# Kernel optimization log

Measured on AMD Instinct MI355X. Metric: run time of the kernel, lower is better.

## Reference

```python
import jax, jax.numpy as jnp
import numpy as np

WH, WW = 8, 8
N_TOK = WH * WW
NUM_HEADS = 4
DIM = 128
B_WIN = 4096  # num_windows * B
NW = 64       # windows per image (for mask)


def _make_rel_tables():
    # relative coords table (1, 2*Wh-1, 2*Ww-1, 2), log-spaced as in SwinV2
    ch = np.arange(-(WH - 1), WH, dtype=np.float32)
    cw = np.arange(-(WW - 1), WW, dtype=np.float32)
    t = np.stack(np.meshgrid(ch, cw, indexing='ij'), axis=-1)[None]  # (1,15,15,2)
    t[..., 0] /= (WH - 1)
    t[..., 1] /= (WW - 1)
    t *= 8
    t = np.sign(t) * np.log2(np.abs(t) + 1.0) / np.log2(8)
    # relative position index (N, N)
    coords = np.stack(np.meshgrid(np.arange(WH), np.arange(WW), indexing='ij'))
    cf = coords.reshape(2, -1)
    rel = cf[:, :, None] - cf[:, None, :]
    rel = rel.transpose(1, 2, 0).copy()
    rel[:, :, 0] += WH - 1
    rel[:, :, 1] += WW - 1
    rel[:, :, 0] *= 2 * WW - 1
    idx = rel.sum(-1).astype(np.int32)
    return jnp.asarray(t), jnp.asarray(idx)


def setup_inputs() -> dict:
    key = jax.random.key(0)
    ks = jax.random.split(key, 8)
    table, idx = _make_rel_tables()
    return {
        'x': jax.random.normal(ks[0], (B_WIN, N_TOK, DIM), jnp.float32),
        'context': jax.random.normal(ks[1], (B_WIN, N_TOK, DIM), jnp.float32),
        'mask': jnp.zeros((NW, N_TOK, N_TOK), jnp.float32),
        'q_w': jax.random.normal(ks[2], (DIM, DIM), jnp.float32) * 0.02,
        'q_b': jnp.zeros((DIM,), jnp.float32),
        'kv_w': jax.random.normal(ks[3], (2 * DIM, DIM), jnp.float32) * 0.02,
        'v_b': jnp.zeros((DIM,), jnp.float32),
        'logit_scale': jnp.full((NUM_HEADS, 1, 1), np.log(10.0), jnp.float32),
        'cpb_w1': jax.random.normal(ks[4], (512, 2), jnp.float32) * 0.02,
        'cpb_b1': jnp.zeros((512,), jnp.float32),
        'cpb_w2': jax.random.normal(ks[5], (NUM_HEADS, 512), jnp.float32) * 0.02,
        'proj_w': jax.random.normal(ks[6], (DIM, DIM), jnp.float32) * 0.02,
        'proj_b': jnp.zeros((DIM,), jnp.float32),
        'rel_coords_table': table,
        'rel_pos_index': idx,
    }


def _l2norm(t, eps=1e-12):
    return t / jnp.maximum(jnp.linalg.norm(t, axis=-1, keepdims=True), eps)


def reference(x, context, mask, q_w, q_b, kv_w, v_b, logit_scale,
              cpb_w1, cpb_b1, cpb_w2, proj_w, proj_b,
              rel_coords_table, rel_pos_index):
    B_, N, C = x.shape
    H = NUM_HEADS
    hd = C // H
    # projections (kv bias = [zeros_like(v_b); v_b])
    q = x @ q_w.T + q_b
    kv_bias = jnp.concatenate([jnp.zeros_like(v_b), v_b])
    kv = context @ kv_w.T + kv_bias
    q = q.reshape(B_, N, H, hd).transpose(0, 2, 1, 3)          # (B_,H,N,hd)
    kv = kv.reshape(B_, N, 2, H, hd).transpose(2, 0, 3, 1, 4)  # (2,B_,H,N,hd)
    k, v = kv[0], kv[1]
    # cosine attention with clamped learned scale
    attn = jnp.einsum('bhnd,bhmd->bhnm', _l2norm(q), _l2norm(k))
    scale = jnp.exp(jnp.minimum(logit_scale, np.log(1.0 / 0.01)))  # (H,1,1)
    attn = attn * scale[None]
    # CPB-MLP relative position bias
    hidd = jax.nn.relu(rel_coords_table @ cpb_w1.T + cpb_b1)   # (1,15,15,512)
    table = (hidd @ cpb_w2.T).reshape(-1, H)                   # ((2Wh-1)(2Ww-1), H)
    bias = table[rel_pos_index.reshape(-1)].reshape(N, N, H)
    bias = 16.0 * jax.nn.sigmoid(bias.transpose(2, 0, 1))      # (H,N,N)
    attn = attn + bias[None]
    # shift mask
    nW = mask.shape[0]
    attn = attn.reshape(B_ // nW, nW, H, N, N) + mask[None, :, None]
    attn = attn.reshape(B_, H, N, N)
    attn = jax.nn.softmax(attn, axis=-1)
    out = jnp.einsum('bhnm,bhmd->bhnd', attn, v)
    out = out.transpose(0, 2, 1, 3).reshape(B_, N, C)
    return out @ proj_w.T + proj_b
```

## Files before the change

kernel.cpp:

```cpp
#include <hip/hip_runtime.h>
#include <hip/hip_bf16.h>

#define NT 64
#define DIM 128
#define NH 4
#define HD 32

typedef __attribute__((ext_vector_type(8))) short short8;
typedef __attribute__((ext_vector_type(4))) short short4v;
typedef __attribute__((ext_vector_type(8))) __bf16 bf16x8;
typedef __attribute__((ext_vector_type(4))) float floatx4;

__device__ __forceinline__ short f2bf(float f) {
  unsigned u = __builtin_bit_cast(unsigned, f);
  u += 0x7FFFu + ((u >> 16) & 1u);
  return (short)(u >> 16);
}

__device__ __forceinline__ bf16x8 ldsfrag(const short* p) {
  return __builtin_bit_cast(bf16x8, *(const short8*)p);
}

#define MFMA(a,b,c) __builtin_amdgcn_mfma_f32_16x16x32_bf16(a,b,c,0,0,0)

__global__ void prep_kernel(const float* __restrict__ table,
                            const float* __restrict__ w1,
                            const float* __restrict__ b1,
                            const float* __restrict__ w2,
                            const int*   __restrict__ idx,
                            const float* __restrict__ q_w,
                            const float* __restrict__ kv_w,
                            const float* __restrict__ proj_w,
                            float* __restrict__ bias_packed,
                            short* __restrict__ wbf) {
  int t = threadIdx.x;
  if (blockIdx.x == 0) {
    __shared__ float logits[225][4];
    if (t < 225) {
      float t0 = table[2*t], t1 = table[2*t+1];
      float a0=0.f, a1=0.f, a2=0.f, a3=0.f;
      for (int j = 0; j < 512; ++j) {
        float h = fmaxf(0.f, t0 * w1[2*j] + t1 * w1[2*j+1] + b1[j]);
        a0 += h * w2[j];
        a1 += h * w2[512 + j];
        a2 += h * w2[1024 + j];
        a3 += h * w2[1536 + j];
      }
      logits[t][0]=a0; logits[t][1]=a1; logits[t][2]=a2; logits[t][3]=a3;
    }
    __syncthreads();
    for (int f = t; f < 16384; f += 256) {
      int i    = f & 3;
      int lane = (f >> 2) & 63;
      int nt   = (f >> 8) & 3;
      int mt   = (f >> 10) & 3;
      int h    = (f >> 12) & 3;
      int r = mt*16 + (lane >> 4)*4 + i;
      int c = nt*16 + (lane & 15);
      int p = idx[r*64 + c];
      float v = logits[p][h];
      bias_packed[f] = 16.f / (1.f + __expf(-v));
    }
  } else {
    int gidx = (blockIdx.x - 1) * 4096 + t * 16;
    const float* src; int off;
    if (gidx < 16384)      { src = q_w;    off = gidx; }
    else if (gidx < 49152) { src = kv_w;   off = gidx - 16384; }
    else                   { src = proj_w; off = gidx - 49152; }
    const float4* s = (const float4*)(src + off);
    short* dst = wbf + gidx;
#pragma unroll
    for (int i = 0; i < 2; ++i) {
      float4 a = s[2*i], b = s[2*i+1];
      short8 v;
      v[0]=f2bf(a.x); v[1]=f2bf(a.y); v[2]=f2bf(a.z); v[3]=f2bf(a.w);
      v[4]=f2bf(b.x); v[5]=f2bf(b.y); v[6]=f2bf(b.z); v[7]=f2bf(b.w);
      *(short8*)(dst + i*8) = v;
    }
  }
}

__global__ __launch_bounds__(512, 4)
void swin_ctx_attn_kernel(const float* __restrict__ x, const float* __restrict__ ctx,
                          const float* __restrict__ mask,
                          const short* __restrict__ wq, const float* __restrict__ q_b,
                          const short* __restrict__ wkv, const float* __restrict__ v_b,
                          const float* __restrict__ logit_scale,
                          const short* __restrict__ wproj, const float* __restrict__ proj_b,
                          const float* __restrict__ bias_p,
                          float* __restrict__ out) {
  __shared__ short lds[38400] __attribute__((aligned(16)));
  const int tid  = threadIdx.x;
  const int lane = tid & 63;
  const int wv   = tid >> 6;
  const int h    = wv >> 1;
  const int s    = wv & 1;
  const int b    = blockIdx.x;
  const int lr   = lane & 15;
  const int lg   = lane >> 4;

  short* stage = lds;
  short* hb    = lds + 8704 + h * 7424;
  short* qn    = hb;
  short* kn    = hb + 2560;
  short* attnb = hb;
  short* vT    = hb + 5120;

  const int sr = tid >> 3, sc = (tid & 7) * 16;
  {
    const float4* sx = (const float4*)(x + (size_t)b * (NT*DIM) + sr*DIM + sc);
    short* d = stage + sr*136 + sc;
#pragma unroll
    for (int i = 0; i < 2; ++i) {
      float4 a = sx[2*i], bb = sx[2*i+1];
      short8 v;
      v[0]=f2bf(a.x); v[1]=f2bf(a.y); v[2]=f2bf(a.z); v[3]=f2bf(a.w);
      v[4]=f2bf(bb.x); v[5]=f2bf(bb.y); v[6]=f2bf(bb.z); v[7]=f2bf(bb.w);
      *(short8*)(d + i*8) = v;
    }
  }
  float4 cr[4];
  {
    const float4* cs = (const float4*)(ctx + (size_t)b * (NT*DIM) + sr*DIM + sc);
#pragma unroll
    for (int i = 0; i < 4; ++i) cr[i] = cs[i];
  }
  __syncthreads();

  {
    floatx4 acc[2][2] = {};
    for (int ks = 0; ks < 4; ++ks) {
      bf16x8 A[2];
#pragma unroll
      for (int m = 0; m < 2; ++m)
        A[m] = ldsfrag(stage + (s*32 + m*16 + lr)*136 + ks*32 + lg*8);
#pragma unroll
      for (int nt = 0; nt < 2; ++nt) {
        bf16x8 B = ldsfrag(wq + (h*32 + nt*16 + lr)*DIM + ks*32 + lg*8);
#pragma unroll
        for (int m = 0; m < 2; ++m)
          acc[m][nt] = MFMA(A[m], B, acc[m][nt]);
      }
    }
    float qb0 = q_b[h*32 + lr], qb1 = q_b[h*32 + 16 + lr];
#pragma unroll
    for (int m = 0; m < 2; ++m) {
      floatx4 ss;
#pragma unroll
      for (int i = 0; i < 4; ++i) {
        acc[m][0][i] += qb0; acc[m][1][i] += qb1;
        ss[i] = acc[m][0][i]*acc[m][0][i] + acc[m][1][i]*acc[m][1][i];
      }
      for (int mm = 1; mm < 16; mm <<= 1)
#pragma unroll
        for (int i = 0; i < 4; ++i) ss[i] += __shfl_xor(ss[i], mm, 64);
#pragma unroll
      for (int i = 0; i < 4; ++i) {
        float sc2 = 1.0f / fmaxf(sqrtf(ss[i]), 1e-12f);
        int row = s*32 + m*16 + lg*4 + i;
        qn[row*40 + lr]      = f2bf(acc[m][0][i] * sc2);
        qn[row*40 + 16 + lr] = f2bf(acc[m][1][i] * sc2);
      }
    }
  }
  __syncthreads();

  {
    short* d = stage + sr*136 + sc;
#pragma unroll
    for (int i = 0; i < 2; ++i) {
      float4 a = cr[2*i], bb = cr[2*i+1];
      short8 v;
      v[0]=f2bf(a.x); v[1]=f2bf(a.y); v[2]=f2bf(a.z); v[3]=f2bf(a.w);
      v[4]=f2bf(bb.x); v[5]=f2bf(bb.y); v[6]=f2bf(bb.z); v[7]=f2bf(bb.w);
      *(short8*)(d + i*8) = v;
    }
  }
  __syncthreads();

  {
    floatx4 acc[2][2] = {};
    for (int ks = 0; ks < 4; ++ks) {
      bf16x8 A[2];
#pragma unroll
      for (int m = 0; m < 2; ++m)
        A[m] = ldsfrag(stage + (s*32 + m*16 + lr)*136 + ks*32 + lg*8);
#pragma unroll
      for (int nt = 0; nt < 2; ++nt) {
        bf16x8 B = ldsfrag(wkv + (h*32 + nt*16 + lr)*DIM + ks*32 + lg*8);
#pragma unroll
        for (int m = 0; m < 2; ++m)
          acc[m][nt] = MFMA(A[m], B, acc[m][nt]);
      }
    }
#pragma unroll
    for (int m = 0; m < 2; ++m) {
      floatx4 ss;
#pragma unroll
      for (int i = 0; i < 4; ++i)
        ss[i] = acc[m][0][i]*acc[m][0][i] + acc[m][1][i]*acc[m][1][i];
      for (int mm = 1; mm < 16; mm <<= 1)
#pragma unroll
        for (int i = 0; i < 4; ++i) ss[i] += __shfl_xor(ss[i], mm, 64);
#pragma unroll
      for (int i = 0; i < 4; ++i) {
        float sc2 = 1.0f / fmaxf(sqrtf(ss[i]), 1e-12f);
        int row = s*32 + m*16 + lg*4 + i;
        kn[row*40 + lr]      = f2bf(acc[m][0][i] * sc2);
        kn[row*40 + 16 + lr] = f2bf(acc[m][1][i] * sc2);
      }
    }
  }

  {
    floatx4 acc[2][2] = {};
    for (int ks = 0; ks < 4; ++ks) {
      bf16x8 A[2];
#pragma unroll
      for (int m = 0; m < 2; ++m)
        A[m] = ldsfrag(stage + (s*32 + m*16 + lr)*136 + ks*32 + lg*8);
#pragma unroll
      for (int nt = 0; nt < 2; ++nt) {
        bf16x8 B = ldsfrag(wkv + (DIM + h*32 + nt*16 + lr)*DIM + ks*32 + lg*8);
#pragma unroll
        for (int m = 0; m < 2; ++m)
          acc[m][nt] = MFMA(A[m], B, acc[m][nt]);
      }
    }
    float vb0 = v_b[h*32 + lr], vb1 = v_b[h*32 + 16 + lr];
#pragma unroll
    for (int m = 0; m < 2; ++m)
#pragma unroll
      for (int nt = 0; nt < 2; ++nt) {
        float vb = nt ? vb1 : vb0;
        short4v s4;
#pragma unroll
        for (int i = 0; i < 4; ++i) s4[i] = f2bf(acc[m][nt][i] + vb);
        *(short4v*)(vT + (nt*16 + lr)*72 + s*32 + m*16 + lg*4) = s4;
      }
  }
  __syncthreads();

  floatx4 sacc[2][4] = {};
  {
    bf16x8 A[2];
#pragma unroll
    for (int m = 0; m < 2; ++m)
      A[m] = ldsfrag(qn + (s*32 + m*16 + lr)*40 + lg*8);
#pragma unroll
    for (int nt = 0; nt < 4; ++nt) {
      bf16x8 B = ldsfrag(kn + (nt*16 + lr)*40 + lg*8);
#pragma unroll
      for (int m = 0; m < 2; ++m)
        sacc[m][nt] = MFMA(A[m], B, sacc[m][nt]);
    }
  }
  __syncthreads();

  {
    float scl = __expf(fminf(logit_scale[h], 4.605170185988091f));
    int wimg = b & 63;
#pragma unroll
    for (int m = 0; m < 2; ++m)
#pragma unroll
      for (int nt = 0; nt < 4; ++nt) {
        floatx4 bias4 = ((const floatx4*)bias_p)[(h*16 + (s*2+m)*4 + nt)*64 + lane];
#pragma unroll
        for (int i = 0; i < 4; ++i) {
          int r = s*32 + m*16 + lg*4 + i, c = nt*16 + lr;
          sacc[m][nt][i] = sacc[m][nt][i]*scl + bias4[i] + mask[((size_t)wimg*64 + r)*64 + c];
        }
      }
#pragma unroll
    for (int m = 0; m < 2; ++m) {
      floatx4 rmax;
#pragma unroll
      for (int i = 0; i < 4; ++i)
        rmax[i] = fmaxf(fmaxf(sacc[m][0][i], sacc[m][1][i]), fmaxf(sacc[m][2][i], sacc[m][3][i]));
      for (int mm = 1; mm < 16; mm <<= 1)
#pragma unroll
        for (int i = 0; i < 4; ++i) rmax[i] = fmaxf(rmax[i], __shfl_xor(rmax[i], mm, 64));
      floatx4 rsum = {};
#pragma unroll
      for (int nt = 0; nt < 4; ++nt)
#pragma unroll
        for (int i = 0; i < 4; ++i) {
          sacc[m][nt][i] = __expf(sacc[m][nt][i] - rmax[i]);
          rsum[i] += sacc[m][nt][i];
        }
      for (int mm = 1; mm < 16; mm <<= 1)
#pragma unroll
        for (int i = 0; i < 4; ++i) rsum[i] += __shfl_xor(rsum[i], mm, 64);
#pragma unroll
      for (int i = 0; i < 4; ++i) rsum[i] = 1.0f / rsum[i];
#pragma unroll
      for (int nt = 0; nt < 4; ++nt)
#pragma unroll
        for (int i = 0; i < 4; ++i) sacc[m][nt][i] *= rsum[i];
    }
  }

#pragma unroll
  for (int m = 0; m < 2; ++m)
#pragma unroll
    for (int nt = 0; nt < 4; ++nt)
#pragma unroll
      for (int i = 0; i < 4; ++i)
        attnb[(s*32 + m*16 + lg*4 + i)*72 + nt*16 + lr] = f2bf(sacc[m][nt][i]);
  asm volatile("s_waitcnt lgkmcnt(0)" ::: "memory");

  floatx4 oacc[2][2] = {};
  for (int ks = 0; ks < 2; ++ks) {
    bf16x8 A[2];
#pragma unroll
    for (int m = 0; m < 2; ++m)
      A[m] = ldsfrag(attnb + (s*32 + m*16 + lr)*72 + ks*32 + lg*8);
#pragma unroll
    for (int nt = 0; nt < 2; ++nt) {
      bf16x8 B = ldsfrag(vT + (nt*16 + lr)*72 + ks*32 + lg*8);
#pragma unroll
      for (int m = 0; m < 2; ++m)
        oacc[m][nt] = MFMA(A[m], B, oacc[m][nt]);
    }
  }

#pragma unroll
  for (int m = 0; m < 2; ++m)
#pragma unroll
    for (int nt = 0; nt < 2; ++nt)
#pragma unroll
      for (int i = 0; i < 4; ++i)
        stage[(s*32 + m*16 + lg*4 + i)*136 + h*32 + nt*16 + lr] = f2bf(oacc[m][nt][i]);
  __syncthreads();

  {
    floatx4 acc[2][2] = {};
    for (int ks = 0; ks < 4; ++ks) {
      bf16x8 A[2];
#pragma unroll
      for (int m = 0; m < 2; ++m)
        A[m] = ldsfrag(stage + (s*32 + m*16 + lr)*136 + ks*32 + lg*8);
#pragma unroll
      for (int nt = 0; nt < 2; ++nt) {
        bf16x8 B = ldsfrag(wproj + (h*32 + nt*16 + lr)*DIM + ks*32 + lg*8);
#pragma unroll
        for (int m = 0; m < 2; ++m)
          acc[m][nt] = MFMA(A[m], B, acc[m][nt]);
      }
    }
    float pb0 = proj_b[h*32 + lr], pb1 = proj_b[h*32 + 16 + lr];
    float* outp = out + (size_t)b * (NT*DIM);
#pragma unroll
    for (int m = 0; m < 2; ++m)
#pragma unroll
      for (int nt = 0; nt < 2; ++nt) {
        float pb = nt ? pb1 : pb0;
#pragma unroll
        for (int i = 0; i < 4; ++i)
          outp[(s*32 + m*16 + lg*4 + i)*DIM + h*32 + nt*16 + lr] = acc[m][nt][i] + pb;
      }
  }
}

extern "C" void kernel_launch(void* const* d_in, const int* in_sizes, int n_in,
                              void* d_out, int out_size, void* d_ws, size_t ws_size,
                              hipStream_t stream) {
  const float* x     = (const float*)d_in[0];
  const float* ctx   = (const float*)d_in[1];
  const float* mask  = (const float*)d_in[2];
  const float* q_w   = (const float*)d_in[3];
  const float* q_b   = (const float*)d_in[4];
  const float* kv_w  = (const float*)d_in[5];
  const float* v_b   = (const float*)d_in[6];
  const float* ls    = (const float*)d_in[7];
  const float* w1    = (const float*)d_in[8];
  const float* b1    = (const float*)d_in[9];
  const float* w2    = (const float*)d_in[10];
  const float* pw    = (const float*)d_in[11];
  const float* pb    = (const float*)d_in[12];
  const float* table = (const float*)d_in[13];
  const int*   idx   = (const int*)d_in[14];

  float* bias_p = (float*)d_ws;
  short* wbf    = (short*)((char*)d_ws + 65536);
  short* wq     = wbf;
  short* wkv    = wbf + 16384;
  short* wproj  = wbf + 49152;
  int B = in_sizes[0] / (NT * DIM);

  prep_kernel<<<17, 256, 0, stream>>>(table, w1, b1, w2, idx, q_w, kv_w, pw,
                                      bias_p, wbf);
  swin_ctx_attn_kernel<<<B, 512, 0, stream>>>(x, ctx, mask, wq, q_b, wkv, v_b,
                                              ls, wproj, pb, bias_p, (float*)d_out);
}
```

Measured before the change: 273.1 us.

## Load x/ctx fragments directly from global, fuse K/V GEMMs, swizzle LDS

Removes the LDS staging of x and context. Each wave now loads its fp32 A fragments straight from global memory and converts them to bf16 in registers. The K and V projections share one k-loop over a single A load, several syncs are dropped, and all LDS buffers use an XOR swizzle instead of padding, which shrinks shared memory enough to raise the occupancy target from 4 to 6. The trade-off is redundant global reads of x and ctx across the four head-waves, plus higher register pressure under the tighter launch bound.

```diff
diff --git a/kernel.cpp b/kernel.cpp
--- a/kernel.cpp
+++ b/kernel.cpp
@@ -3,25 +3,31 @@
 
 #define NT 64
 #define DIM 128
-#define NH 4
-#define HD 32
 
 typedef __attribute__((ext_vector_type(8))) short short8;
 typedef __attribute__((ext_vector_type(4))) short short4v;
 typedef __attribute__((ext_vector_type(8))) __bf16 bf16x8;
 typedef __attribute__((ext_vector_type(4))) float floatx4;
 
-__device__ __forceinline__ short f2bf(float f) {
-  unsigned u = __builtin_bit_cast(unsigned, f);
-  u += 0x7FFFu + ((u >> 16) & 1u);
-  return (short)(u >> 16);
-}
-
-__device__ __forceinline__ bf16x8 ldsfrag(const short* p) {
+#define MFMA(a,b,c) __builtin_amdgcn_mfma_f32_16x16x32_bf16(a,b,c,0,0,0)
+#define SWZ(idx, row) ((idx) ^ (((row)&7)<<3))
+
+__device__ __forceinline__ short bfbits(float f) {
+  return __builtin_bit_cast(short, (__bf16)f);
+}
+
+__device__ __forceinline__ bf16x8 gfrag_f32(const float* __restrict__ p) {
+  float4 a = *(const float4*)p;
+  float4 b = *(const float4*)(p + 4);
+  bf16x8 v;
+  v[0]=(__bf16)a.x; v[1]=(__bf16)a.y; v[2]=(__bf16)a.z; v[3]=(__bf16)a.w;
+  v[4]=(__bf16)b.x; v[5]=(__bf16)b.y; v[6]=(__bf16)b.z; v[7]=(__bf16)b.w;
+  return v;
+}
+
+__device__ __forceinline__ bf16x8 frag_bf(const short* __restrict__ p) {
   return __builtin_bit_cast(bf16x8, *(const short8*)p);
 }
-
-#define MFMA(a,b,c) __builtin_amdgcn_mfma_f32_16x16x32_bf16(a,b,c,0,0,0)
 
 __global__ void prep_kernel(const float* __restrict__ table,
                             const float* __restrict__ w1,
@@ -73,14 +79,14 @@
     for (int i = 0; i < 2; ++i) {
       float4 a = s[2*i], b = s[2*i+1];
       short8 v;
-      v[0]=f2bf(a.x); v[1]=f2bf(a.y); v[2]=f2bf(a.z); v[3]=f2bf(a.w);
-      v[4]=f2bf(b.x); v[5]=f2bf(b.y); v[6]=f2bf(b.z); v[7]=f2bf(b.w);
+      v[0]=bfbits(a.x); v[1]=bfbits(a.y); v[2]=bfbits(a.z); v[3]=bfbits(a.w);
+      v[4]=bfbits(b.x); v[5]=bfbits(b.y); v[6]=bfbits(b.z); v[7]=bfbits(b.w);
       *(short8*)(dst + i*8) = v;
     }
   }
 }
 
-__global__ __launch_bounds__(512, 4)
+__global__ __launch_bounds__(512, 6)
 void swin_ctx_attn_kernel(const float* __restrict__ x, const float* __restrict__ ctx,
                           const float* __restrict__ mask,
                           const short* __restrict__ wq, const float* __restrict__ q_b,
@@ -89,7 +95,7 @@
                           const short* __restrict__ wproj, const float* __restrict__ proj_b,
                           const float* __restrict__ bias_p,
                           float* __restrict__ out) {
-  __shared__ short lds[38400] __attribute__((aligned(16)));
+  __shared__ short lds[24576] __attribute__((aligned(16)));
   const int tid  = threadIdx.x;
   const int lane = tid & 63;
   const int wv   = tid >> 6;
@@ -99,48 +105,30 @@
   const int lr   = lane & 15;
   const int lg   = lane >> 4;
 
-  short* stage = lds;
-  short* hb    = lds + 8704 + h * 7424;
-  short* qn    = hb;
-  short* kn    = hb + 2560;
-  short* attnb = hb;
-  short* vT    = hb + 5120;
-
-  const int sr = tid >> 3, sc = (tid & 7) * 16;
-  {
-    const float4* sx = (const float4*)(x + (size_t)b * (NT*DIM) + sr*DIM + sc);
-    short* d = stage + sr*136 + sc;
-#pragma unroll
-    for (int i = 0; i < 2; ++i) {
-      float4 a = sx[2*i], bb = sx[2*i+1];
-      short8 v;
-      v[0]=f2bf(a.x); v[1]=f2bf(a.y); v[2]=f2bf(a.z); v[3]=f2bf(a.w);
-      v[4]=f2bf(bb.x); v[5]=f2bf(bb.y); v[6]=f2bf(bb.z); v[7]=f2bf(bb.w);
-      *(short8*)(d + i*8) = v;
-    }
-  }
-  float4 cr[4];
-  {
-    const float4* cs = (const float4*)(ctx + (size_t)b * (NT*DIM) + sr*DIM + sc);
-#pragma unroll
-    for (int i = 0; i < 4; ++i) cr[i] = cs[i];
-  }
-  __syncthreads();
+  short* qn     = lds + h*6144;
+  short* kn     = qn + 2048;
+  short* vT     = qn + 4096;
+  short* attnb  = qn;
+  short* outp_l = lds;
+
+  const float* xw = x   + (size_t)b*(NT*DIM);
+  const float* cw = ctx + (size_t)b*(NT*DIM);
 
   {
     floatx4 acc[2][2] = {};
     for (int ks = 0; ks < 4; ++ks) {
-      bf16x8 A[2];
+      bf16x8 A[2], B[2];
 #pragma unroll
       for (int m = 0; m < 2; ++m)
-        A[m] = ldsfrag(stage + (s*32 + m*16 + lr)*136 + ks*32 + lg*8);
-#pragma unroll
-      for (int nt = 0; nt < 2; ++nt) {
-        bf16x8 B = ldsfrag(wq + (h*32 + nt*16 + lr)*DIM + ks*32 + lg*8);
+        A[m] = gfrag_f32(xw + (s*32 + m*16 + lr)*DIM + ks*32 + lg*8);
+#pragma unroll
+      for (int n = 0; n < 2; ++n)
+        B[n] = frag_bf(wq + (h*32 + n*16 + lr)*DIM + ks*32 + lg*8);
+#pragma unroll
+      for (int n = 0; n < 2; ++n)
 #pragma unroll
         for (int m = 0; m < 2; ++m)
-          acc[m][nt] = MFMA(A[m], B, acc[m][nt]);
-      }
+          acc[m][n] = MFMA(A[m], B[n], acc[m][n]);
     }
     float qb0 = q_b[h*32 + lr], qb1 = q_b[h*32 + 16 + lr];
 #pragma unroll
@@ -156,106 +144,85 @@
         for (int i = 0; i < 4; ++i) ss[i] += __shfl_xor(ss[i], mm, 64);
 #pragma unroll
       for (int i = 0; i < 4; ++i) {
-        float sc2 = 1.0f / fmaxf(sqrtf(ss[i]), 1e-12f);
+        float sc = 1.0f / fmaxf(sqrtf(ss[i]), 1e-12f);
         int row = s*32 + m*16 + lg*4 + i;
-        qn[row*40 + lr]      = f2bf(acc[m][0][i] * sc2);
-        qn[row*40 + 16 + lr] = f2bf(acc[m][1][i] * sc2);
-      }
-    }
+        qn[SWZ(row*32 + lr,      row)] = bfbits(acc[m][0][i] * sc);
+        qn[SWZ(row*32 + 16 + lr, row)] = bfbits(acc[m][1][i] * sc);
+      }
+    }
+  }
+
+  {
+    floatx4 kacc[2][2] = {}, vacc[2][2] = {};
+    for (int ks = 0; ks < 4; ++ks) {
+      bf16x8 A[2], Bk[2], Bv[2];
+#pragma unroll
+      for (int m = 0; m < 2; ++m)
+        A[m] = gfrag_f32(cw + (s*32 + m*16 + lr)*DIM + ks*32 + lg*8);
+#pragma unroll
+      for (int n = 0; n < 2; ++n) {
+        Bk[n] = frag_bf(wkv + (h*32 + n*16 + lr)*DIM + ks*32 + lg*8);
+        Bv[n] = frag_bf(wkv + (DIM + h*32 + n*16 + lr)*DIM + ks*32 + lg*8);
+      }
+#pragma unroll
+      for (int n = 0; n < 2; ++n)
+#pragma unroll
+        for (int m = 0; m < 2; ++m) {
+          kacc[m][n] = MFMA(A[m], Bk[n], kacc[m][n]);
+          vacc[m][n] = MFMA(A[m], Bv[n], vacc[m][n]);
+        }
+    }
+#pragma unroll
+    for (int m = 0; m < 2; ++m) {
+      floatx4 ss;
+#pragma unroll
+      for (int i = 0; i < 4; ++i)
+        ss[i] = kacc[m][0][i]*kacc[m][0][i] + kacc[m][1][i]*kacc[m][1][i];
+      for (int mm = 1; mm < 16; mm <<= 1)
+#pragma unroll
+        for (int i = 0; i < 4; ++i) ss[i] += __shfl_xor(ss[i], mm, 64);
+#pragma unroll
+      for (int i = 0; i < 4; ++i) {
+        float sc = 1.0f / fmaxf(sqrtf(ss[i]), 1e-12f);
+        int row = s*32 + m*16 + lg*4 + i;
+        kn[SWZ(row*32 + lr,      row)] = bfbits(kacc[m][0][i] * sc);
+        kn[SWZ(row*32 + 16 + lr, row)] = bfbits(kacc[m][1][i] * sc);
+      }
+    }
+    float vb0 = v_b[h*32 + lr], vb1 = v_b[h*32 + 16 + lr];
+#pragma unroll
+    for (int m = 0; m < 2; ++m)
+#pragma unroll
+      for (int n = 0; n < 2; ++n) {
+        float vb = n ? vb1 : vb0;
+        short4v s4;
+#pragma unroll
+        for (int i = 0; i < 4; ++i) s4[i] = bfbits(vacc[m][n][i] + vb);
+        int d = n*16 + lr, tok0 = s*32 + m*16 + lg*4;
+        *(short4v*)(vT + SWZ(d*64 + tok0, d)) = s4;
+      }
   }
   __syncthreads();
 
-  {
-    short* d = stage + sr*136 + sc;
-#pragma unroll
-    for (int i = 0; i < 2; ++i) {
-      float4 a = cr[2*i], bb = cr[2*i+1];
-      short8 v;
-      v[0]=f2bf(a.x); v[1]=f2bf(a.y); v[2]=f2bf(a.z); v[3]=f2bf(a.w);
-      v[4]=f2bf(bb.x); v[5]=f2bf(bb.y); v[6]=f2bf(bb.z); v[7]=f2bf(bb.w);
-      *(short8*)(d + i*8) = v;
-    }
-  }
-  __syncthreads();
-
-  {
-    floatx4 acc[2][2] = {};
-    for (int ks = 0; ks < 4; ++ks) {
-      bf16x8 A[2];
+  floatx4 sacc[2][4] = {};
+  {
+    bf16x8 A[2], Bf[4];
+#pragma unroll
+    for (int m = 0; m < 2; ++m) {
+      int q = s*32 + m*16 + lr;
+      A[m] = frag_bf(qn + SWZ(q*32 + lg*8, q));
+    }
+#pragma unroll
+    for (int n = 0; n < 4; ++n) {
+      int r = n*16 + lr;
+      Bf[n] = frag_bf(kn + SWZ(r*32 + lg*8, r));
+    }
+#pragma unroll
+    for (int n = 0; n < 4; ++n)
 #pragma unroll
       for (int m = 0; m < 2; ++m)
-        A[m] = ldsfrag(stage + (s*32 + m*16 + lr)*136 + ks*32 + lg*8);
-#pragma unroll
-      for (int nt = 0; nt < 2; ++nt) {
-        bf16x8 B = ldsfrag(wkv + (h*32 + nt*16 + lr)*DIM + ks*32 + lg*8);
-#pragma unroll
-        for (int m = 0; m < 2; ++m)
-          acc[m][nt] = MFMA(A[m], B, acc[m][nt]);
-      }
-    }
-#pragma unroll
-    for (int m = 0; m < 2; ++m) {
-      floatx4 ss;
-#pragma unroll
-      for (int i = 0; i < 4; ++i)
-        ss[i] = acc[m][0][i]*acc[m][0][i] + acc[m][1][i]*acc[m][1][i];
-      for (int mm = 1; mm < 16; mm <<= 1)
-#pragma unroll
-        for (int i = 0; i < 4; ++i) ss[i] += __shfl_xor(ss[i], mm, 64);
-#pragma unroll
-      for (int i = 0; i < 4; ++i) {
-        float sc2 = 1.0f / fmaxf(sqrtf(ss[i]), 1e-12f);
-        int row = s*32 + m*16 + lg*4 + i;
-        kn[row*40 + lr]      = f2bf(acc[m][0][i] * sc2);
-        kn[row*40 + 16 + lr] = f2bf(acc[m][1][i] * sc2);
-      }
-    }
-  }
-
-  {
-    floatx4 acc[2][2] = {};
-    for (int ks = 0; ks < 4; ++ks) {
-      bf16x8 A[2];
-#pragma unroll
-      for (int m = 0; m < 2; ++m)
-        A[m] = ldsfrag(stage + (s*32 + m*16 + lr)*136 + ks*32 + lg*8);
-#pragma unroll
-      for (int nt = 0; nt < 2; ++nt) {
-        bf16x8 B = ldsfrag(wkv + (DIM + h*32 + nt*16 + lr)*DIM + ks*32 + lg*8);
-#pragma unroll
-        for (int m = 0; m < 2; ++m)
-          acc[m][nt] = MFMA(A[m], B, acc[m][nt]);
-      }
-    }
-    float vb0 = v_b[h*32 + lr], vb1 = v_b[h*32 + 16 + lr];
-#pragma unroll
-    for (int m = 0; m < 2; ++m)
-#pragma unroll
-      for (int nt = 0; nt < 2; ++nt) {
-        float vb = nt ? vb1 : vb0;
-        short4v s4;
-#pragma unroll
-        for (int i = 0; i < 4; ++i) s4[i] = f2bf(acc[m][nt][i] + vb);
-        *(short4v*)(vT + (nt*16 + lr)*72 + s*32 + m*16 + lg*4) = s4;
-      }
-  }
-  __syncthreads();
-
-  floatx4 sacc[2][4] = {};
-  {
-    bf16x8 A[2];
-#pragma unroll
-    for (int m = 0; m < 2; ++m)
-      A[m] = ldsfrag(qn + (s*32 + m*16 + lr)*40 + lg*8);
-#pragma unroll
-    for (int nt = 0; nt < 4; ++nt) {
-      bf16x8 B = ldsfrag(kn + (nt*16 + lr)*40 + lg*8);
-#pragma unroll
-      for (int m = 0; m < 2; ++m)
-        sacc[m][nt] = MFMA(A[m], B, sacc[m][nt]);
-    }
-  }
-  __syncthreads();
+        sacc[m][n] = MFMA(A[m], Bf[n], sacc[m][n]);
+  }
 
   {
     float scl = __expf(fminf(logit_scale[h], 4.605170185988091f));
@@ -299,65 +266,81 @@
         for (int i = 0; i < 4; ++i) sacc[m][nt][i] *= rsum[i];
     }
   }
+  __syncthreads();
 
 #pragma unroll
   for (int m = 0; m < 2; ++m)
 #pragma unroll
     for (int nt = 0; nt < 4; ++nt)
 #pragma unroll
-      for (int i = 0; i < 4; ++i)
-        attnb[(s*32 + m*16 + lg*4 + i)*72 + nt*16 + lr] = f2bf(sacc[m][nt][i]);
+      for (int i = 0; i < 4; ++i) {
+        int q = s*32 + m*16 + lg*4 + i;
+        attnb[SWZ(q*64 + nt*16 + lr, q)] = bfbits(sacc[m][nt][i]);
+      }
   asm volatile("s_waitcnt lgkmcnt(0)" ::: "memory");
+  __builtin_amdgcn_sched_barrier(0);
 
   floatx4 oacc[2][2] = {};
+#pragma unroll
   for (int ks = 0; ks < 2; ++ks) {
-    bf16x8 A[2];
-#pragma unroll
-    for (int m = 0; m < 2; ++m)
-      A[m] = ldsfrag(attnb + (s*32 + m*16 + lr)*72 + ks*32 + lg*8);
-#pragma unroll
-    for (int nt = 0; nt < 2; ++nt) {
-      bf16x8 B = ldsfrag(vT + (nt*16 + lr)*72 + ks*32 + lg*8);
+    bf16x8 A[2], Bf[2];
+#pragma unroll
+    for (int m = 0; m < 2; ++m) {
+      int q = s*32 + m*16 + lr;
+      A[m] = frag_bf(attnb + SWZ(q*64 + ks*32 + lg*8, q));
+    }
+#pragma unroll
+    for (int n = 0; n < 2; ++n) {
+      int d = n*16 + lr;
+      Bf[n] = frag_bf(vT + SWZ(d*64 + ks*32 + lg*8, d));
+    }
+#pragma unroll
+    for (int n = 0; n < 2; ++n)
 #pragma unroll
       for (int m = 0; m < 2; ++m)
-        oacc[m][nt] = MFMA(A[m], B, oacc[m][nt]);
-    }
-  }
+        oacc[m][n] = MFMA(A[m], Bf[n], oacc[m][n]);
+  }
+  __syncthreads();
 
 #pragma unroll
   for (int m = 0; m < 2; ++m)
 #pragma unroll
-    for (int nt = 0; nt < 2; ++nt)
-#pragma unroll
-      for (int i = 0; i < 4; ++i)
-        stage[(s*32 + m*16 + lg*4 + i)*136 + h*32 + nt*16 + lr] = f2bf(oacc[m][nt][i]);
+    for (int n = 0; n < 2; ++n)
+#pragma unroll
+      for (int i = 0; i < 4; ++i) {
+        int q = s*32 + m*16 + lg*4 + i;
+        outp_l[SWZ(q*128 + h*32 + n*16 + lr, q)] = bfbits(oacc[m][n][i]);
+      }
   __syncthreads();
 
   {
     floatx4 acc[2][2] = {};
     for (int ks = 0; ks < 4; ++ks) {
-      bf16x8 A[2];
-#pragma unroll
-      for (int m = 0; m < 2; ++m)
-        A[m] = ldsfrag(stage + (s*32 + m*16 + lr)*136 + ks*32 + lg*8);
-#pragma unroll
-      for (int nt = 0; nt < 2; ++nt) {
-        bf16x8 B = ldsfrag(wproj + (h*32 + nt*16 + lr)*DIM + ks*32 + lg*8);
+      bf16x8 A[2], B[2];
+#pragma unroll
+      for (int m = 0; m < 2; ++m) {
+        int q = s*32 + m*16 + lr;
+        A[m] = frag_bf(outp_l + SWZ(q*128 + ks*32 + lg*8, q));
+      }
+#pragma unroll
+      for (int n = 0; n < 2; ++n)
+        B[n] = frag_bf(wproj + (h*32 + n*16 + lr)*DIM + ks*32 + lg*8);
+#pragma unroll
+      for (int n = 0; n < 2; ++n)
 #pragma unroll
         for (int m = 0; m < 2; ++m)
-          acc[m][nt] = MFMA(A[m], B, acc[m][nt]);
-      }
+          acc[m][n] = MFMA(A[m], B[n], acc[m][n]);
     }
     float pb0 = proj_b[h*32 + lr], pb1 = proj_b[h*32 + 16 + lr];
     float* outp = out + (size_t)b * (NT*DIM);
 #pragma unroll
     for (int m = 0; m < 2; ++m)
 #pragma unroll
-      for (int nt = 0; nt < 2; ++nt) {
-        float pb = nt ? pb1 : pb0;
+      for (int n = 0; n < 2; ++n) {
+        float pb = n ? pb1 : pb0;
 #pragma unroll
         for (int i = 0; i < 4; ++i)
-          outp[(s*32 + m*16 + lg*4 + i)*DIM + h*32 + nt*16 + lr] = acc[m][nt][i] + pb;
+          outp[(s*32 + m*16 + lg*4 + i)*DIM + h*32 + n*16 + lr] = acc[m][n][i] + pb;
       }
   }
 }
```

Measured after the change: 420.8 us. 54.1% more time.
